# Kernel tuning notes

Hardware: AMD Instinct MI355X
Metric: run time of the kernel (lower is better)

## Reference

```python
import jax, jax.numpy as jnp
import numpy as np

D_MODEL = 1024
N_HEADS = 16
D_HEAD = D_MODEL // N_HEADS


def setup_inputs() -> dict:
    key = jax.random.key(0)
    k1, k2, k3 = jax.random.split(key, 3)
    B, T = 2, 2048
    x = jax.random.normal(k1, (B, T, D_MODEL), dtype=jnp.float32)
    # kaiming_normal fan_out on torch Linear weight [out, in]: std = sqrt(2/out)
    qkv_w = jax.random.normal(k2, (3 * D_MODEL, D_MODEL), dtype=jnp.float32) * np.sqrt(2.0 / (3 * D_MODEL)).astype(np.float32)
    out_w = jax.random.normal(k3, (D_MODEL, D_MODEL), dtype=jnp.float32) * np.sqrt(2.0 / D_MODEL).astype(np.float32)
    return {"x": x, "qkv_w": qkv_w, "out_w": out_w}


def rotate_half(x):
    x1, x2 = x[..., : x.shape[-1] // 2], x[..., x.shape[-1] // 2 :]
    return jnp.concatenate((-x2, x1), axis=-1)


def reference(x, qkv_w, out_w):
    B, T, D = x.shape
    H, dh = N_HEADS, D_HEAD
    scale = dh ** -0.5

    qkv = jnp.einsum('btd,ed->bte', x, qkv_w)  # [B,T,3D]
    q, k, v = jnp.split(qkv, 3, axis=-1)
    # [B,H,T,dh]
    q = q.reshape(B, T, H, dh).transpose(0, 2, 1, 3)
    k = k.reshape(B, T, H, dh).transpose(0, 2, 1, 3)
    v = v.reshape(B, T, H, dh).transpose(0, 2, 1, 3)

    # rotary embeddings
    inv_freq = 1.0 / (10000.0 ** (jnp.arange(0, dh, 2, dtype=jnp.float32) / dh))
    t = jnp.arange(T, dtype=jnp.float32)
    freqs = jnp.einsum('i,j->ij', t, inv_freq)        # [T, dh/2]
    emb = jnp.concatenate((freqs, freqs), axis=-1)    # [T, dh]
    cos = jnp.cos(emb)[None, None]                    # [1,1,T,dh]
    sin = jnp.sin(emb)[None, None]
    q = q * cos + rotate_half(q) * sin
    k = k * cos + rotate_half(k) * sin

    scores = jnp.einsum('bhqd,bhkd->bhqk', q, k) * scale
    causal = jnp.tril(jnp.ones((T, T), dtype=bool))
    scores = jnp.where(causal, scores, -jnp.inf)
    attn = jax.nn.softmax(scores, axis=-1)
    out = jnp.einsum('bhqk,bhkd->bhqd', attn, v)      # [B,H,T,dh]
    out = out.transpose(0, 2, 1, 3).reshape(B, T, D)
    return jnp.einsum('btd,ed->bte', out, out_w)
```

## Files before the change

### kernel.cpp

```cpp
#include <hip/hip_runtime.h>
#include <hip/hip_bf16.h>
#include <cmath>

#define Bb   2
#define Tseq 2048
#define NH   16
#define DM   1024

using f32x4 = __attribute__((ext_vector_type(4))) float;
using s16x8 = __attribute__((ext_vector_type(8))) short;
using s16x4 = __attribute__((ext_vector_type(4))) short;

typedef const __attribute__((address_space(1))) unsigned char* as1p;
typedef __attribute__((address_space(3))) unsigned char* as3p;

static __device__ __forceinline__ void gload_lds16(const void* g, void* l){
  __builtin_amdgcn_global_load_lds((as1p)g, (as3p)l, 16, 0, 0);
}

#if defined(__has_builtin)
#if __has_builtin(__builtin_amdgcn_mfma_f32_16x16x16bf16_1k)
#define MFMA16(acc, va, pb) (acc) = __builtin_amdgcn_mfma_f32_16x16x16bf16_1k((va), (pb), (acc), 0, 0, 0)
#endif
#endif
#ifndef MFMA16
#define MFMA16(acc, va, pb) asm volatile("s_nop 1\n\tv_mfma_f32_16x16x16_bf16 %0, %1, %2, %0" : "+v"(acc) : "v"(va), "v"(pb))
#endif

static __device__ __forceinline__ float b2f(unsigned short u){
  union { unsigned int u; float f; } v; v.u = ((unsigned int)u) << 16; return v.f;
}
static __device__ __forceinline__ unsigned short f2b(float f){
  union { float f; unsigned int u; } v; v.f = f;
  unsigned int u = v.u;
  return (unsigned short)((u + 0x7fffu + ((u >> 16) & 1u)) >> 16);
}

__global__ void k_convert(const float* __restrict__ in, unsigned short* __restrict__ out, int n){
  int stride = gridDim.x * blockDim.x;
  for (int i = blockIdx.x * blockDim.x + threadIdx.x; i * 4 < n; i += stride) {
    const float4 v = *reinterpret_cast<const float4*>(in + (size_t)i * 4);
    ushort4 o; o.x = f2b(v.x); o.y = f2b(v.y); o.z = f2b(v.z); o.w = f2b(v.w);
    *reinterpret_cast<ushort4*>(out + (size_t)i * 4) = o;
  }
}

template<int MODE>
__global__ __launch_bounds__(256) void k_gemm_bt(const unsigned short* __restrict__ A,
                                                 const unsigned short* __restrict__ W,
                                                 void* __restrict__ Cout,
                                                 int M, int N, int K, int NYL,
                                                 unsigned short* __restrict__ qr,
                                                 unsigned short* __restrict__ kr){
  __shared__ unsigned short As[128*64];
  __shared__ unsigned short Bs[128*64];
  const int i = (int)blockIdx.x;
  const int xcd = i & 7, rr = i >> 3;
  const int bx = rr / NYL, by = xcd * NYL + (rr % NYL);
  const int bm = bx * 128, bn = by * 128;
  const int tid = threadIdx.x;
  const int lane = tid & 63, w = tid >> 6;
  const int wr = w >> 1, wc = w & 1;
  const int g = lane >> 4, ln = lane & 15;
  f32x4 acc[4][4] = {};
  char* asb = (char*)As + w * 4096;
  char* bsb = (char*)Bs + w * 4096;
  const int lrow8 = lane >> 3;
  const int kcolb = ((lane & 7) ^ lrow8) * 16;
  const size_t aro = (size_t)(bm + w * 32 + lrow8) * K;
  const size_t bro = (size_t)(bn + w * 32 + lrow8) * K;
  const int xr = (ln & 7) << 4;
  for (int k0 = 0; k0 < K; k0 += 64) {
    #pragma unroll
    for (int q4 = 0; q4 < 4; ++q4) {
      gload_lds16((const char*)(A + aro + (size_t)(q4 * 8) * K + k0) + kcolb, asb + q4 * 1024);
      gload_lds16((const char*)(W + bro + (size_t)(q4 * 8) * K + k0) + kcolb, bsb + q4 * 1024);
    }
    __syncthreads();
    #pragma unroll
    for (int kk = 0; kk < 2; ++kk) {
      s16x8 af[4], bfr[4];
      const int ro = (kk * 64 + g * 16) ^ xr;
      #pragma unroll
      for (int mt = 0; mt < 4; ++mt)
        af[mt] = *reinterpret_cast<const s16x8*>((char*)As + (wr*64 + mt*16 + ln) * 128 + ro);
      #pragma unroll
      for (int nt = 0; nt < 4; ++nt)
        bfr[nt] = *reinterpret_cast<const s16x8*>((char*)Bs + (wc*64 + nt*16 + ln) * 128 + ro);
      #pragma unroll
      for (int mt = 0; mt < 4; ++mt)
        #pragma unroll
        for (int nt = 0; nt < 4; ++nt)
          acc[mt][nt] = __builtin_amdgcn_mfma_f32_16x16x32_bf16(af[mt], bfr[nt], acc[mt][nt], 0, 0, 0);
    }
    __syncthreads();
  }
  if (MODE == 0) {
    #pragma unroll
    for (int mt = 0; mt < 4; ++mt)
      #pragma unroll
      for (int nt = 0; nt < 4; ++nt)
        #pragma unroll
        for (int r = 0; r < 4; ++r) {
          int row = bm + wr*64 + mt*16 + g*4 + r;
          int col = bn + wc*64 + nt*16 + ln;
          reinterpret_cast<float*>(Cout)[(size_t)row * N + col] = acc[mt][nt][r];
        }
  } else {
    const int region = bn >> 10;
    if (region == 2) {
      #pragma unroll
      for (int mt = 0; mt < 4; ++mt)
        #pragma unroll
        for (int nt = 0; nt < 4; ++nt)
          #pragma unroll
          for (int r = 0; r < 4; ++r) {
            int row = bm + wr*64 + mt*16 + g*4 + r;
            int col = bn + wc*64 + nt*16 + ln;
            reinterpret_cast<unsigned short*>(Cout)[(size_t)row * N + col] = f2b(acc[mt][nt][r]);
          }
    } else {
      const float if0 = exp2f(-(float)ln        * 0.4152410118074f);
      const float if1 = exp2f(-(float)(16 + ln) * 0.4152410118074f);
      const int h = ((bn + wc * 64) >> 6) & 15;
      unsigned short* dst = (region == 0) ? qr : kr;
      const float qs = (region == 0) ? 0.125f : 1.0f;
      #pragma unroll
      for (int mt = 0; mt < 4; ++mt)
        #pragma unroll
        for (int r = 0; r < 4; ++r) {
          int row = bm + wr*64 + mt*16 + g*4 + r;
          int t = row & (Tseq - 1), b = row >> 11;
          float c0, s0, c1, s1;
          __sincosf((float)t * if0, &s0, &c0);
          __sincosf((float)t * if1, &s1, &c1);
          float v0 = (acc[mt][0][r] * c0 - acc[mt][2][r] * s0) * qs;
          float v1 = (acc[mt][1][r] * c1 - acc[mt][3][r] * s1) * qs;
          float v2 = (acc[mt][2][r] * c0 + acc[mt][0][r] * s0) * qs;
          float v3 = (acc[mt][3][r] * c1 + acc[mt][1][r] * s1) * qs;
          size_t base = ((size_t)(b * NH + h) * Tseq + t) * 64 + ln;
          dst[base]      = f2b(v0);
          dst[base + 16] = f2b(v1);
          dst[base + 32] = f2b(v2);
          dst[base + 48] = f2b(v3);
        }
    }
  }
}

__global__ __launch_bounds__(256) void k_vtrans(const unsigned short* __restrict__ qkv,
                                                unsigned short* __restrict__ vt){
  __shared__ unsigned short L[64*72];
  const int blk = blockIdx.x;
  const int tt64 = blk & 31, bh = blk >> 5;
  const int b = bh >> 4, h = bh & 15;
  const int t0 = tt64 * 64;
  const int tid = threadIdx.x;
  {
    const int tr = tid >> 2, c = tid & 3;
    const unsigned short* src = qkv + ((size_t)(b * Tseq) + t0 + tr) * 3072 + 2048 + h * 64 + c * 16;
    uint4 a0 = *reinterpret_cast<const uint4*>(src);
    uint4 a1 = *reinterpret_cast<const uint4*>(src + 8);
    *reinterpret_cast<uint4*>(&L[tr * 72 + c * 16])     = a0;
    *reinterpret_cast<uint4*>(&L[tr * 72 + c * 16 + 8]) = a1;
  }
  __syncthreads();
  {
    const int d = tid >> 2, c = tid & 3;
    unsigned int wq[8];
    #pragma unroll
    for (int j = 0; j < 8; ++j) {
      unsigned int lo = L[(c * 16 + 2 * j)     * 72 + d];
      unsigned int hi = L[(c * 16 + 2 * j + 1) * 72 + d];
      wq[j] = lo | (hi << 16);
    }
    unsigned short* dst = vt + ((size_t)bh * 64 + d) * Tseq + t0 + c * 16;
    *reinterpret_cast<uint4*>(dst)     = make_uint4(wq[0], wq[1], wq[2], wq[3]);
    *reinterpret_cast<uint4*>(dst + 8) = make_uint4(wq[4], wq[5], wq[6], wq[7]);
  }
}

__global__ __launch_bounds__(256, 2) void k_attn(const unsigned short* __restrict__ Qr,
                                                 const unsigned short* __restrict__ Kr,
                                                 const unsigned short* __restrict__ Vt,
                                                 unsigned short* __restrict__ Ao){
  __shared__ unsigned short Ks[2][64*64];
  __shared__ unsigned short Vs[2][64*64];
  __shared__ unsigned short Ps[4][16*72];
  const int i = (int)blockIdx.x;
  const int xcd = i & 7, r = i >> 3;
  const int bh = xcd * 4 + (r >> 4);
  const int pj = r & 15;
  const unsigned short* Q  = Qr + (size_t)bh * Tseq * 64;
  const unsigned short* Kp = Kr + (size_t)bh * Tseq * 64;
  const unsigned short* Vp = Vt + (size_t)bh * 64 * Tseq;
  const int tid = threadIdx.x;
  const int w = tid >> 6, lane = tid & 63;
  const int g = lane >> 4, ln = lane & 15;
  const int srow = tid >> 2;
  const int c2 = (tid & 3) * 2;
  const int wb0 = srow * 128 + ((c2 * 16)        ^ ((srow & 7) << 4));
  const int wb1 = srow * 128 + ((c2 * 16 + 16)   ^ ((srow & 7) << 4));
  const int scol = c2 * 8;
  const int x0 = (g * 16)      ^ ((ln & 7) << 4);
  const int x1 = (64 + g * 16) ^ ((ln & 7) << 4);
  unsigned short* Pw = Ps[w];
  const int b = bh / NH, h = bh % NH;

  #pragma unroll
  for (int pass = 0; pass < 2; ++pass) {
    const int j = pass ? (31 - pj) : pj;
    const int q0 = j * 64;
    const int ntiles = j + 1;
    const int q0w = q0 + w * 16;

    s16x8 qf0 = *reinterpret_cast<const s16x8*>(&Q[(size_t)(q0w + ln) * 64 + g * 8]);
    s16x8 qf1 = *reinterpret_cast<const s16x8*>(&Q[(size_t)(q0w + ln) * 64 + 32 + g * 8]);

    f32x4 oacc[4] = {};
    float lsum = 0.f;

    {
      uint4 k0 = *reinterpret_cast<const uint4*>(&Kp[(size_t)srow * 64 + scol]);
      uint4 k1 = *reinterpret_cast<const uint4*>(&Kp[(size_t)srow * 64 + scol + 8]);
      uint4 v0 = *reinterpret_cast<const uint4*>(&Vp[(size_t)srow * Tseq + scol]);
      uint4 v1 = *reinterpret_cast<const uint4*>(&Vp[(size_t)srow * Tseq + scol + 8]);
      *reinterpret_cast<uint4*>((char*)Ks[0] + wb0) = k0;
      *reinterpret_cast<uint4*>((char*)Ks[0] + wb1) = k1;
      *reinterpret_cast<uint4*>((char*)Vs[0] + wb0) = v0;
      *reinterpret_cast<uint4*>((char*)Vs[0] + wb1) = v1;
    }
    __syncthreads();
    int cur = 0;

    for (int kt = 0; kt < ntiles; ++kt) {
      const bool pre = (kt + 1 < ntiles);
      uint4 nk0, nk1, nv0, nv1;
      if (pre) {
        const unsigned short* gk = &Kp[(size_t)((kt + 1) * 64 + srow) * 64 + scol];
        const unsigned short* gv = &Vp[(size_t)srow * Tseq + (kt + 1) * 64 + scol];
        nk0 = *reinterpret_cast<const uint4*>(gk);
        nk1 = *reinterpret_cast<const uint4*>(gk + 8);
        nv0 = *reinterpret_cast<const uint4*>(gv);
        nv1 = *reinterpret_cast<const uint4*>(gv + 8);
      }
      f32x4 s[4] = {};
      const char* kb = (const char*)Ks[cur];
      __builtin_amdgcn_s_setprio(1);
      #pragma unroll
      for (int nt = 0; nt < 4; ++nt) {
        s16x8 kfa = *reinterpret_cast<const s16x8*>(kb + nt * 2048 + ln * 128 + x0);
        s16x8 kfb = *reinterpret_cast<const s16x8*>(kb + nt * 2048 + ln * 128 + x1);
        s[nt] = __builtin_amdgcn_mfma_f32_16x16x32_bf16(kfa, qf0, s[nt], 0, 0, 0);
        s[nt] = __builtin_amdgcn_mfma_f32_16x16x32_bf16(kfb, qf1, s[nt], 0, 0, 0);
      }
      __builtin_amdgcn_s_setprio(0);
      if (kt == ntiles - 1) {
        #pragma unroll
        for (int nt = 0; nt < 4; ++nt)
          #pragma unroll
          for (int r2 = 0; r2 < 4; ++r2)
            if (nt * 16 + g * 4 + r2 > w * 16 + ln) s[nt][r2] = -1e30f;
      }
      s16x4 pb[4];
      #pragma unroll
      for (int nt = 0; nt < 4; ++nt)
        #pragma unroll
        for (int r2 = 0; r2 < 4; ++r2) {
          float p = __expf(s[nt][r2]);
          lsum += p;
          pb[nt][r2] = (short)f2b(p);
        }
      const char* vb = (const char*)Vs[cur];
      __builtin_amdgcn_s_setprio(1);
      #pragma unroll
      for (int dt = 0; dt < 4; ++dt) {
        #pragma unroll
        for (int nt = 0; nt < 4; ++nt) {
          s16x4 va = *reinterpret_cast<const s16x4*>(vb + (dt * 16 + ln) * 128 + ((nt * 32 + g * 8) ^ ((ln & 7) << 4)));
          MFMA16(oacc[dt], va, pb[nt]);
        }
      }
      __builtin_amdgcn_s_setprio(0);
      if (pre) {
        const int nxt = cur ^ 1;
        *reinterpret_cast<uint4*>((char*)Ks[nxt] + wb0) = nk0;
        *reinterpret_cast<uint4*>((char*)Ks[nxt] + wb1) = nk1;
        *reinterpret_cast<uint4*>((char*)Vs[nxt] + wb0) = nv0;
        *reinterpret_cast<uint4*>((char*)Vs[nxt] + wb1) = nv1;
      }
      __syncthreads();
      cur ^= 1;
    }

    float l = lsum;
    l += __shfl_xor(l, 16);
    l += __shfl_xor(l, 32);
    float inv = 1.f / l;
    #pragma unroll
    for (int nt = 0; nt < 4; ++nt) {
      unsigned int lo = (unsigned int)f2b(oacc[nt][0] * inv) | ((unsigned int)f2b(oacc[nt][1] * inv) << 16);
      unsigned int hi = (unsigned int)f2b(oacc[nt][2] * inv) | ((unsigned int)f2b(oacc[nt][3] * inv) << 16);
      *reinterpret_cast<uint2*>(&Pw[ln * 72 + nt * 16 + g * 4]) = make_uint2(lo, hi);
    }
    asm volatile("s_waitcnt lgkmcnt(0)" ::: "memory");
    __builtin_amdgcn_sched_barrier(0);
    const int rr = lane >> 2;
    const int cc = (lane & 3) * 8;
    uint4 ov0 = *reinterpret_cast<const uint4*>(&Pw[rr * 72 + cc]);
    uint4 ov1 = *reinterpret_cast<const uint4*>(&Pw[rr * 72 + cc + 32]);
    int t = q0w + rr;
    unsigned short* orow = &Ao[((size_t)(b * Tseq + t) * DM) + h * 64];
    *reinterpret_cast<uint4*>(orow + cc)      = ov0;
    *reinterpret_cast<uint4*>(orow + cc + 32) = ov1;
  }
}

extern "C" void kernel_launch(void* const* d_in, const int* in_sizes, int n_in,
                              void* d_out, int out_size, void* d_ws, size_t ws_size,
                              hipStream_t stream) {
  const float* x    = (const float*)d_in[0];
  const float* qkvw = (const float*)d_in[1];
  const float* outw = (const float*)d_in[2];
  float* out = (float*)d_out;
  char* ws = (char*)d_ws;
  size_t off = 0;
  auto alloc = [&](size_t bytes)->void*{ void* p = ws + off; off += (bytes + 255) & ~(size_t)255; return p; };
  unsigned short* x_bf   = (unsigned short*)alloc((size_t)Bb*Tseq*DM*2);
  unsigned short* qw_bf  = (unsigned short*)alloc((size_t)3*DM*DM*2);
  unsigned short* ow_bf  = (unsigned short*)alloc((size_t)DM*DM*2);
  unsigned short* qkv_bf = (unsigned short*)alloc((size_t)Bb*Tseq*3*DM*2);
  unsigned short* qr     = (unsigned short*)alloc((size_t)Bb*NH*Tseq*64*2);
  unsigned short* kr     = (unsigned short*)alloc((size_t)Bb*NH*Tseq*64*2);
  unsigned short* vt     = (unsigned short*)alloc((size_t)Bb*NH*Tseq*64*2);
  unsigned short* ao     = (unsigned short*)alloc((size_t)Bb*Tseq*DM*2);
  (void)ws_size; (void)in_sizes; (void)n_in; (void)out_size;

  const int nx  = Bb*Tseq*DM;
  const int nqw = 3*DM*DM;
  const int now = DM*DM;
  k_convert<<<2048, 256, 0, stream>>>(x, x_bf, nx);
  k_convert<<<2048, 256, 0, stream>>>(qkvw, qw_bf, nqw);
  k_convert<<<1024, 256, 0, stream>>>(outw, ow_bf, now);
  k_gemm_bt<2><<<768, 256, 0, stream>>>(x_bf, qw_bf, qkv_bf, Bb*Tseq, 3*DM, DM, 3, qr, kr);
  k_vtrans<<<Bb*NH*(Tseq/64), 256, 0, stream>>>(qkv_bf, vt);
  k_attn<<<dim3(Bb*NH*16), 256, 0, stream>>>(qr, kr, vt, ao);
  k_gemm_bt<0><<<256, 256, 0, stream>>>(ao, ow_bf, out, Bb*Tseq, DM, DM, 1, qr, kr);
}
```

Measured before the change: 116.2 us.

## Load K tiles via direct global-to-LDS, swizzle V stores, use exp2 softmax

K tiles are now moved into shared memory with global_load_lds (direct DMA) instead of passing through registers, using a new XOR-swizzled layout. V stores are split into 8-byte pieces with an extended swizzle to reduce bank conflicts on the 4-element reads. The Q scale folds log2(e) in so softmax can use exp2f, and P is converted to bf16 by truncation rather than rounding. This saves register staging and VALU work, at the cost of slightly lower precision and a new layout whose correctness depends on the K fragment reads matching it.

```diff
diff --git a/kernel.cpp b/kernel.cpp
--- a/kernel.cpp
+++ b/kernel.cpp
@@ -124,7 +124,7 @@
       const float if1 = exp2f(-(float)(16 + ln) * 0.4152410118074f);
       const int h = ((bn + wc * 64) >> 6) & 15;
       unsigned short* dst = (region == 0) ? qr : kr;
-      const float qs = (region == 0) ? 0.125f : 1.0f;
+      const float qs = (region == 0) ? 0.18033688011112042f : 1.0f;
       #pragma unroll
       for (int mt = 0; mt < 4; ++mt)
         #pragma unroll
@@ -197,13 +197,19 @@
   const int tid = threadIdx.x;
   const int w = tid >> 6, lane = tid & 63;
   const int g = lane >> 4, ln = lane & 15;
+  const int klr = lane >> 3;
+  const int klc = ((lane & 7) ^ klr) * 8;
   const int srow = tid >> 2;
   const int c2 = (tid & 3) * 2;
-  const int wb0 = srow * 128 + ((c2 * 16)        ^ ((srow & 7) << 4));
-  const int wb1 = srow * 128 + ((c2 * 16 + 16)   ^ ((srow & 7) << 4));
   const int scol = c2 * 8;
+  const int vswz = ((srow & 7) << 4) | (srow & 8);
+  const int vb0 = srow * 128 + ((c2 * 16)      ^ vswz);
+  const int vb1 = srow * 128 + ((c2 * 16 + 8)  ^ vswz);
+  const int vb2 = srow * 128 + ((c2 * 16 + 16) ^ vswz);
+  const int vb3 = srow * 128 + ((c2 * 16 + 24) ^ vswz);
   const int x0 = (g * 16)      ^ ((ln & 7) << 4);
   const int x1 = (64 + g * 16) ^ ((ln & 7) << 4);
+  const int pvswz = ((ln & 7) << 4) | (ln & 8);
   unsigned short* Pw = Ps[w];
   const int b = bh / NH, h = bh % NH;
 
@@ -221,26 +227,29 @@
     float lsum = 0.f;
 
     {
-      uint4 k0 = *reinterpret_cast<const uint4*>(&Kp[(size_t)srow * 64 + scol]);
-      uint4 k1 = *reinterpret_cast<const uint4*>(&Kp[(size_t)srow * 64 + scol + 8]);
-      uint4 v0 = *reinterpret_cast<const uint4*>(&Vp[(size_t)srow * Tseq + scol]);
-      uint4 v1 = *reinterpret_cast<const uint4*>(&Vp[(size_t)srow * Tseq + scol + 8]);
-      *reinterpret_cast<uint4*>((char*)Ks[0] + wb0) = k0;
-      *reinterpret_cast<uint4*>((char*)Ks[0] + wb1) = k1;
-      *reinterpret_cast<uint4*>((char*)Vs[0] + wb0) = v0;
-      *reinterpret_cast<uint4*>((char*)Vs[0] + wb1) = v1;
+      const unsigned short* gk = Kp + (size_t)(w * 16 + klr) * 64 + klc;
+      gload_lds16(gk,       (char*)Ks[0] + w * 2048);
+      gload_lds16(gk + 512, (char*)Ks[0] + w * 2048 + 1024);
+      const unsigned short* gv = Vp + (size_t)srow * Tseq + scol;
+      uint4 v0 = *reinterpret_cast<const uint4*>(gv);
+      uint4 v1 = *reinterpret_cast<const uint4*>(gv + 8);
+      *reinterpret_cast<uint2*>((char*)Vs[0] + vb0) = make_uint2(v0.x, v0.y);
+      *reinterpret_cast<uint2*>((char*)Vs[0] + vb1) = make_uint2(v0.z, v0.w);
+      *reinterpret_cast<uint2*>((char*)Vs[0] + vb2) = make_uint2(v1.x, v1.y);
+      *reinterpret_cast<uint2*>((char*)Vs[0] + vb3) = make_uint2(v1.z, v1.w);
     }
     __syncthreads();
     int cur = 0;
 
     for (int kt = 0; kt < ntiles; ++kt) {
       const bool pre = (kt + 1 < ntiles);
-      uint4 nk0, nk1, nv0, nv1;
+      const int nxt = cur ^ 1;
+      uint4 nv0, nv1;
       if (pre) {
-        const unsigned short* gk = &Kp[(size_t)((kt + 1) * 64 + srow) * 64 + scol];
-        const unsigned short* gv = &Vp[(size_t)srow * Tseq + (kt + 1) * 64 + scol];
-        nk0 = *reinterpret_cast<const uint4*>(gk);
-        nk1 = *reinterpret_cast<const uint4*>(gk + 8);
+        const unsigned short* gk = Kp + (size_t)((kt + 1) * 64 + w * 16 + klr) * 64 + klc;
+        gload_lds16(gk,       (char*)Ks[nxt] + w * 2048);
+        gload_lds16(gk + 512, (char*)Ks[nxt] + w * 2048 + 1024);
+        const unsigned short* gv = Vp + (size_t)srow * Tseq + (kt + 1) * 64 + scol;
         nv0 = *reinterpret_cast<const uint4*>(gv);
         nv1 = *reinterpret_cast<const uint4*>(gv + 8);
       }
@@ -267,9 +276,9 @@
       for (int nt = 0; nt < 4; ++nt)
         #pragma unroll
         for (int r2 = 0; r2 < 4; ++r2) {
-          float p = __expf(s[nt][r2]);
+          float p = exp2f(s[nt][r2]);
           lsum += p;
-          pb[nt][r2] = (short)f2b(p);
+          pb[nt][r2] = (short)(__float_as_uint(p) >> 16);
         }
       const char* vb = (const char*)Vs[cur];
       __builtin_amdgcn_s_setprio(1);
@@ -277,17 +286,16 @@
       for (int dt = 0; dt < 4; ++dt) {
         #pragma unroll
         for (int nt = 0; nt < 4; ++nt) {
-          s16x4 va = *reinterpret_cast<const s16x4*>(vb + (dt * 16 + ln) * 128 + ((nt * 32 + g * 8) ^ ((ln & 7) << 4)));
+          s16x4 va = *reinterpret_cast<const s16x4*>(vb + (dt * 16 + ln) * 128 + ((nt * 32 + g * 8) ^ pvswz));
           MFMA16(oacc[dt], va, pb[nt]);
         }
       }
       __builtin_amdgcn_s_setprio(0);
       if (pre) {
-        const int nxt = cur ^ 1;
-        *reinterpret_cast<uint4*>((char*)Ks[nxt] + wb0) = nk0;
-        *reinterpret_cast<uint4*>((char*)Ks[nxt] + wb1) = nk1;
-        *reinterpret_cast<uint4*>((char*)Vs[nxt] + wb0) = nv0;
-        *reinterpret_cast<uint4*>((char*)Vs[nxt] + wb1) = nv1;
+        *reinterpret_cast<uint2*>((char*)Vs[nxt] + vb0) = make_uint2(nv0.x, nv0.y);
+        *reinterpret_cast<uint2*>((char*)Vs[nxt] + vb1) = make_uint2(nv0.z, nv0.w);
+        *reinterpret_cast<uint2*>((char*)Vs[nxt] + vb2) = make_uint2(nv1.x, nv1.y);
+        *reinterpret_cast<uint2*>((char*)Vs[nxt] + vb3) = make_uint2(nv1.z, nv1.w);
       }
       __syncthreads();
       cur ^= 1;
```

After: 129.4 us. +11.4%, slower.
